# Optimization experiments

Measured on AMD Instinct MI355X. Metric: run time of the kernel, lower is better.

Reference implementation:

```python
import jax, jax.numpy as jnp
import numpy as np

B, T, C, H = 2, 2048, 1024, 16
HD = C // H
HID = C * 4 // 3  # 1365, SwiGLU hidden
EPS = 1e-5


def _ln(x, g, b):
    m = x.mean(-1, keepdims=True)
    v = ((x - m) ** 2).mean(-1, keepdims=True)
    return (x - m) / jnp.sqrt(v + EPS) * g + b


def setup_inputs() -> dict:
    key0 = jax.random.key(0)
    ks = jax.random.split(key0, 16)
    s = 0.02
    inp = {
        'query': jax.random.normal(ks[0], (B, T, C), jnp.float32),
        'key': jax.random.normal(ks[1], (B, T, C), jnp.float32),
        'g_q': jnp.ones((C,), jnp.float32), 'b_q': jnp.zeros((C,), jnp.float32),
        'g_k': jnp.ones((C,), jnp.float32), 'b_k': jnp.zeros((C,), jnp.float32),
        'in_proj_w': jax.random.normal(ks[2], (3 * C, C), jnp.float32) * s,
        'in_proj_b': jnp.zeros((3 * C,), jnp.float32),
        'out_w': jax.random.normal(ks[3], (C, C), jnp.float32) * s,
        'out_b': jnp.zeros((C,), jnp.float32),
        'proj_w': jax.random.normal(ks[4], (C, C), jnp.float32) * s,
        'proj_b': jnp.zeros((C,), jnp.float32),
        'rel_table': jax.random.normal(ks[5], (H, 2 * 2048 - 1), jnp.float32) * s,
        'g_ffn': jnp.ones((C,), jnp.float32), 'b_ffn': jnp.zeros((C,), jnp.float32),
        'w1': jax.random.normal(ks[6], (HID, C), jnp.float32) * s,
        'w2': jax.random.normal(ks[7], (HID, C), jnp.float32) * s,
        'w3': jax.random.normal(ks[8], (C, HID), jnp.float32) * s,
        'g_out': jnp.ones((C,), jnp.float32), 'b_out': jnp.zeros((C,), jnp.float32),
        'max_len': 2048,
    }
    return inp


def reference(query, key, g_q, b_q, g_k, b_k, in_proj_w, in_proj_b, out_w, out_b,
              proj_w, proj_b, rel_table, g_ffn, b_ffn, w1, w2, w3, g_out, b_out, max_len):
    Tq, Tk = query.shape[1], key.shape[1]
    q = _ln(query, g_q, b_q)
    k = _ln(key, g_k, b_k)
    # in-projection (torch MHA packed weights)
    wq, wk, wv = jnp.split(in_proj_w, 3, axis=0)
    bq, bk, bv = jnp.split(in_proj_b, 3, axis=0)
    qp = (q @ wq.T + bq).reshape(B, Tq, H, HD).transpose(0, 2, 1, 3)
    kp = (k @ wk.T + bk).reshape(B, Tk, H, HD).transpose(0, 2, 1, 3)
    vp = (k @ wv.T + bv).reshape(B, Tk, H, HD).transpose(0, 2, 1, 3)
    # relative-position bias, mean over heads -> [Tq,Tk] additive mask
    rel_idx = jnp.clip(jnp.arange(Tq)[:, None] - jnp.arange(Tk)[None, :] + (max_len - 1),
                       0, 2 * max_len - 2)
    mask = rel_table[:, rel_idx].mean(axis=0)  # [Tq,Tk]
    scores = jnp.einsum('bhqd,bhkd->bhqk', qp, kp) / jnp.sqrt(jnp.float32(HD))
    attn = jax.nn.softmax(scores + mask[None, None], axis=-1)
    ctx = jnp.einsum('bhqk,bhkd->bhqd', attn, vp)
    ctx = ctx.transpose(0, 2, 1, 3).reshape(B, Tq, C)
    attn_out = ctx @ out_w.T + out_b
    attn_out = attn_out @ proj_w.T + proj_b
    x = query + attn_out
    # SwiGLU FFN (proj dropout/dropout are identity at eval)
    h = _ln(x, g_ffn, b_ffn)
    ff = (jax.nn.silu(h @ w1.T) * (h @ w2.T)) @ w3.T
    x = x + ff
    return _ln(x, g_out, b_out)
```

## Files before the change

### kernel.cpp

```cpp
#include <hip/hip_runtime.h>
#include <hip/hip_bf16.h>

static constexpr int Bb  = 2;
static constexpr int Tt  = 2048;
static constexpr int Cc  = 1024;
static constexpr int Hh  = 16;
static constexpr int HDi = 64;
static constexpr int HID = 1365;
static constexpr int HIDP = 1408;
static constexpr int Mm  = Bb * Tt;

typedef unsigned short u16;
typedef __attribute__((ext_vector_type(8))) short bf16x8;
typedef __attribute__((ext_vector_type(4))) float f32x4;
typedef __attribute__((ext_vector_type(8))) unsigned short u16x8;
typedef __attribute__((ext_vector_type(4))) unsigned short u16x4;

__device__ inline u16 f2bf(float f) {
    unsigned u = __builtin_bit_cast(unsigned, f);
    u += 0x7fffu + ((u >> 16) & 1u);
    return (u16)(u >> 16);
}

__device__ inline unsigned cvtpk(float lo, float hi) {
    unsigned r;
    asm("v_cvt_pk_bf16_f32 %0, %1, %2" : "=v"(r) : "v"(lo), "v"(hi));
    return r;
}

__device__ inline float vexp2(float x) {
    float r;
    asm("v_exp_f32 %0, %1" : "=v"(r) : "v"(x));
    return r;
}

__device__ inline void gl16(const void* g, void* l) {
    __builtin_amdgcn_global_load_lds(
        (const __attribute__((address_space(1))) unsigned*)g,
        (__attribute__((address_space(3))) unsigned*)l, 16, 0, 0);
}

template<int OUTBF>
__global__ __launch_bounds__(256) void ln_k(const float* __restrict__ x,
                                            const float* __restrict__ g,
                                            const float* __restrict__ b,
                                            void* __restrict__ yv) {
    int row = blockIdx.x;
    int tid = threadIdx.x;
    const float4* xr = (const float4*)(x + (size_t)row * Cc);
    float4 v = xr[tid];
    float s  = v.x + v.y + v.z + v.w;
    float ss = v.x*v.x + v.y*v.y + v.z*v.z + v.w*v.w;
    __shared__ float rs[256], rq[256];
    rs[tid] = s; rq[tid] = ss;
    __syncthreads();
    for (int o = 128; o > 0; o >>= 1) {
        if (tid < o) { rs[tid] += rs[tid+o]; rq[tid] += rq[tid+o]; }
        __syncthreads();
    }
    float mean = rs[0] * (1.f/Cc);
    float var  = rq[0] * (1.f/Cc) - mean*mean;
    float inv  = rsqrtf(var + 1e-5f);
    float4 gv = ((const float4*)g)[tid];
    float4 bv = ((const float4*)b)[tid];
    float o0 = (v.x-mean)*inv*gv.x + bv.x;
    float o1 = (v.y-mean)*inv*gv.y + bv.y;
    float o2 = (v.z-mean)*inv*gv.z + bv.z;
    float o3 = (v.w-mean)*inv*gv.w + bv.w;
    if (OUTBF) {
        u16x4 o4 = { f2bf(o0), f2bf(o1), f2bf(o2), f2bf(o3) };
        ((u16x4*)((u16*)yv + (size_t)row * Cc))[tid] = o4;
    } else {
        float4 o4 = { o0, o1, o2, o3 };
        ((float4*)((float*)yv + (size_t)row * Cc))[tid] = o4;
    }
}

__global__ __launch_bounds__(256) void ln2_k(const float* __restrict__ q,
                                             const float* __restrict__ k,
                                             const float* __restrict__ gq, const float* __restrict__ bq,
                                             const float* __restrict__ gk, const float* __restrict__ bk,
                                             u16* __restrict__ qn, u16* __restrict__ kn) {
    int row = blockIdx.x;
    const float* x; const float* g; const float* bb; u16* y; int r;
    if (row < Mm) { x = q; g = gq; bb = bq; y = qn; r = row; }
    else          { x = k; g = gk; bb = bk; y = kn; r = row - Mm; }
    int tid = threadIdx.x;
    float4 v = ((const float4*)(x + (size_t)r * Cc))[tid];
    float s  = v.x + v.y + v.z + v.w;
    float ss = v.x*v.x + v.y*v.y + v.z*v.z + v.w*v.w;
    __shared__ float rs[256], rq2[256];
    rs[tid] = s; rq2[tid] = ss;
    __syncthreads();
    for (int o = 128; o > 0; o >>= 1) {
        if (tid < o) { rs[tid] += rs[tid+o]; rq2[tid] += rq2[tid+o]; }
        __syncthreads();
    }
    float mean = rs[0] * (1.f/Cc);
    float var  = rq2[0] * (1.f/Cc) - mean*mean;
    float inv  = rsqrtf(var + 1e-5f);
    float4 gv = ((const float4*)g)[tid];
    float4 bv = ((const float4*)bb)[tid];
    u16x4 o4 = { f2bf((v.x-mean)*inv*gv.x + bv.x), f2bf((v.y-mean)*inv*gv.y + bv.y),
                 f2bf((v.z-mean)*inv*gv.z + bv.z), f2bf((v.w-mean)*inv*gv.w + bv.w) };
    ((u16x4*)(y + (size_t)r * Cc))[tid] = o4;
}

__global__ __launch_bounds__(256) void meanrel_k(const float* __restrict__ rel,
                                                 float* __restrict__ mr) {
    int j = blockIdx.x * 256 + threadIdx.x;
    if (j < 2*Tt - 1) {
        float s = 0.f;
        #pragma unroll
        for (int h = 0; h < Hh; h++) s += rel[(size_t)h * (2*Tt - 1) + j];
        mr[j] = s * (1.f/Hh);
    }
}

__global__ __launch_bounds__(256) void cvt4_k(const float* __restrict__ s0, u16* __restrict__ d0, int n0,
                                              const float* __restrict__ s1, u16* __restrict__ d1, int n1,
                                              const float* __restrict__ s2, u16* __restrict__ d2, int n2, int v2,
                                              const float* __restrict__ s3, u16* __restrict__ d3, int n3, int v3) {
    int u = blockIdx.x * 256 + threadIdx.x;
    const float* src; u16* dst; int valid;
    if (u < n0)              { src = s0; dst = d0; valid = n0*8; }
    else if ((u -= n0) < n1) { src = s1; dst = d1; valid = n1*8; }
    else if ((u -= n1) < n2) { src = s2; dst = d2; valid = v2; }
    else if ((u -= n2) < n3) { src = s3; dst = d3; valid = v3; }
    else return;
    int e0 = u * 8;
    u16x8 o;
    if (e0 + 8 <= valid) {
        float4 a = *(const float4*)(src + e0);
        float4 b = *(const float4*)(src + e0 + 4);
        o[0]=f2bf(a.x); o[1]=f2bf(a.y); o[2]=f2bf(a.z); o[3]=f2bf(a.w);
        o[4]=f2bf(b.x); o[5]=f2bf(b.y); o[6]=f2bf(b.z); o[7]=f2bf(b.w);
    } else {
        #pragma unroll
        for (int j = 0; j < 8; j++) {
            int e = e0 + j;
            o[j] = f2bf(e < valid ? src[e] : 0.f);
        }
    }
    *(u16x8*)(dst + (size_t)e0) = o;
}

__global__ __launch_bounds__(256) void cvt_k(const float* __restrict__ src,
                                             u16* __restrict__ dst,
                                             int Rs, int Cs, int Cd, int total8) {
    int idx = blockIdx.x * 256 + threadIdx.x;
    if (idx >= total8) return;
    int e0 = idx * 8;
    int r = e0 / Cd, c0 = e0 - r * Cd;
    u16x8 o;
    #pragma unroll
    for (int j = 0; j < 8; j++) {
        int c = c0 + j;
        float v = (r < Rs && c < Cs) ? src[(size_t)r * Cs + c] : 0.f;
        o[j] = f2bf(v);
    }
    *(u16x8*)(dst + (size_t)e0) = o;
}

__global__ __launch_bounds__(256) void cvtT_k(const float* __restrict__ src,
                                              u16* __restrict__ dst) {
    __shared__ float t[64][65];
    int j0 = blockIdx.x * 64, c0 = blockIdx.y * 64;
    int tid = threadIdx.x;
    #pragma unroll
    for (int i = 0; i < 16; i++) {
        int e = tid + i*256;
        int c = e >> 6, j = e & 63;
        t[c][j] = src[(size_t)(c0 + c) * Cc + j0 + j];
    }
    __syncthreads();
    #pragma unroll
    for (int i = 0; i < 16; i++) {
        int e = tid + i*256;
        int j = e >> 6, c = e & 63;
        dst[(size_t)(j0 + j) * Cc + c0 + c] = f2bf(t[c][j]);
    }
}

__global__ __launch_bounds__(256) void bias_k(const float* __restrict__ wp,
                                              const float* __restrict__ bo,
                                              const float* __restrict__ bp,
                                              float* __restrict__ bc) {
    int i = blockIdx.x, tid = threadIdx.x;
    float4 w = ((const float4*)(wp + (size_t)i * Cc))[tid];
    float4 b = ((const float4*)bo)[tid];
    float s = w.x*b.x + w.y*b.y + w.z*b.z + w.w*b.w;
    __shared__ float red[256];
    red[tid] = s; __syncthreads();
    for (int o = 128; o > 0; o >>= 1) {
        if (tid < o) red[tid] += red[tid+o];
        __syncthreads();
    }
    if (tid == 0) bc[i] = red[0] + bp[i];
}

template<int OUTBF, int HASRES, int HASBIAS>
__global__ __launch_bounds__(256) void mgemm64_k(const u16* __restrict__ A,
                                                 const u16* __restrict__ W,
                                                 const float* __restrict__ bias,
                                                 const float* __restrict__ res,
                                                 void* __restrict__ outv,
                                                 int N, int K) {
    __shared__ u16 As[2][64*32];
    __shared__ u16 Ws[2][128*32];
    int bm = blockIdx.y * 64, bn = blockIdx.x * 128;
    int tid = threadIdx.x, w = tid >> 6, l = tid & 63;
    int lr = l & 15, lh = l >> 4;
    int wm = (w >> 1) * 32, wn = (w & 1) * 64;
    f32x4 acc[2][4] = {};

    auto stage = [&](int buf, int kt) {
        {
            int row = tid >> 2, slot = tid & 3;
            int ko = kt + ((slot ^ (row & 3)) << 3);
            gl16(A + (size_t)(bm + row) * K + ko, (char*)As[buf] + tid * 16);
        }
        #pragma unroll
        for (int c = 0; c < 2; c++) {
            int i = c*256 + tid;
            int row = i >> 2, slot = i & 3;
            int ko = kt + ((slot ^ (row & 3)) << 3);
            gl16(W + (size_t)(bn + row) * K + ko, (char*)Ws[buf] + (c*256 + tid) * 16);
        }
    };
    stage(0, 0);
    for (int kt = 0; kt < K; kt += 32) {
        int buf = (kt >> 5) & 1;
        __syncthreads();
        if (kt + 32 < K) stage(buf ^ 1, kt + 32);
        bf16x8 af[2], wf[4];
        #pragma unroll
        for (int f = 0; f < 2; f++) {
            int r = wm + f*16 + lr;
            af[f] = *(const bf16x8*)((const char*)As[buf] + r*64 + ((lh ^ (r & 3)) << 4));
        }
        #pragma unroll
        for (int f = 0; f < 4; f++) {
            int rn = wn + f*16 + lr;
            wf[f] = *(const bf16x8*)((const char*)Ws[buf] + rn*64 + ((lh ^ (rn & 3)) << 4));
        }
        #pragma unroll
        for (int fm = 0; fm < 2; fm++)
            #pragma unroll
            for (int fn = 0; fn < 4; fn++)
                acc[fm][fn] = __builtin_amdgcn_mfma_f32_16x16x32_bf16(af[fm], wf[fn], acc[fm][fn], 0, 0, 0);
    }

    #pragma unroll
    for (int fm = 0; fm < 2; fm++) {
        #pragma unroll
        for (int r = 0; r < 4; r++) {
            int row = bm + wm + fm*16 + lh*4 + r;
            #pragma unroll
            for (int fn = 0; fn < 4; fn++) {
                int col = bn + wn + fn*16 + lr;
                float v = acc[fm][fn][r];
                if (HASBIAS) v += bias[col];
                if (HASRES)  v += res[(size_t)row * N + col];
                if (OUTBF) ((u16*)outv)[(size_t)row * N + col] = f2bf(v);
                else       ((float*)outv)[(size_t)row * N + col] = v;
            }
        }
    }
}

__global__ __launch_bounds__(256) void mqkv_k(const u16* __restrict__ qn,
                                              const u16* __restrict__ kn,
                                              const u16* __restrict__ wA,
                                              const float* __restrict__ bias3,
                                              u16* __restrict__ out3) {
    int z = blockIdx.z;
    const u16* A = z ? kn : qn;
    const u16* W = wA + (size_t)z * Cc * Cc;
    const float* bias = bias3 + z * Cc;
    u16* out = out3 + (size_t)z * Mm * Cc;

    __shared__ u16 As[2][128*32];
    __shared__ u16 Ws[2][128*32];
    int bm = blockIdx.y * 128, bn = blockIdx.x * 128;
    int tid = threadIdx.x, w = tid >> 6, l = tid & 63;
    int lr = l & 15, lh = l >> 4;
    int wm = (w >> 1) * 64, wn = (w & 1) * 64;
    f32x4 acc[4][4] = {};

    auto stage = [&](int buf, int kt) {
        #pragma unroll
        for (int c = 0; c < 2; c++) {
            int i = w*128 + c*64 + l;
            int row = i >> 2, slot = i & 3;
            int ko = kt + ((slot ^ (row & 3)) << 3);
            gl16(A + (size_t)(bm + row) * Cc + ko, (char*)As[buf] + (w*128 + c*64) * 16);
            gl16(W + (size_t)(bn + row) * Cc + ko, (char*)Ws[buf] + (w*128 + c*64) * 16);
        }
    };
    stage(0, 0);
    for (int kt = 0; kt < Cc; kt += 32) {
        int buf = (kt >> 5) & 1;
        __syncthreads();
        if (kt + 32 < Cc) stage(buf ^ 1, kt + 32);
        bf16x8 af[4], wf[4];
        #pragma unroll
        for (int f = 0; f < 4; f++) {
            int r = wm + f*16 + lr;
            af[f] = *(const bf16x8*)((const char*)As[buf] + r*64 + ((lh ^ (r & 3)) << 4));
            int rn = wn + f*16 + lr;
            wf[f] = *(const bf16x8*)((const char*)Ws[buf] + rn*64 + ((lh ^ (rn & 3)) << 4));
        }
        #pragma unroll
        for (int fm = 0; fm < 4; fm++)
            #pragma unroll
            for (int fn = 0; fn < 4; fn++)
                acc[fm][fn] = __builtin_amdgcn_mfma_f32_16x16x32_bf16(af[fm], wf[fn], acc[fm][fn], 0, 0, 0);
    }

    #pragma unroll
    for (int fm = 0; fm < 4; fm++) {
        #pragma unroll
        for (int r = 0; r < 4; r++) {
            int row = bm + wm + fm*16 + lh*4 + r;
            #pragma unroll
            for (int fn = 0; fn < 4; fn++) {
                int col = bn + wn + fn*16 + lr;
                out[(size_t)row * Cc + col] = f2bf(acc[fm][fn][r] + bias[col]);
            }
        }
    }
}

__global__ __launch_bounds__(256) void mswiglu64_k(const u16* __restrict__ A,
                                                   const u16* __restrict__ W1,
                                                   const u16* __restrict__ W2,
                                                   u16* __restrict__ out,
                                                   int N, int K) {
    __shared__ u16 As[2][64*32];
    __shared__ u16 W1s[2][128*32];
    __shared__ u16 W2s[2][128*32];
    int bm = blockIdx.y * 64, bn = blockIdx.x * 128;
    int tid = threadIdx.x, w = tid >> 6, l = tid & 63;
    int lr = l & 15, lh = l >> 4;
    int wm = (w >> 1) * 32, wn = (w & 1) * 64;
    f32x4 acc1[2][4] = {};
    f32x4 acc2[2][4] = {};

    auto stage = [&](int buf, int kt) {
        {
            int row = tid >> 2, slot = tid & 3;
            int ko = kt + ((slot ^ (row & 3)) << 3);
            gl16(A + (size_t)(bm + row) * K + ko, (char*)As[buf] + tid * 16);
        }
        #pragma unroll
        for (int c = 0; c < 2; c++) {
            int i = c*256 + tid;
            int row = i >> 2, slot = i & 3;
            int ko = kt + ((slot ^ (row & 3)) << 3);
            gl16(W1 + (size_t)(bn + row) * K + ko, (char*)W1s[buf] + (c*256 + tid) * 16);
            gl16(W2 + (size_t)(bn + row) * K + ko, (char*)W2s[buf] + (c*256 + tid) * 16);
        }
    };
    stage(0, 0);
    for (int kt = 0; kt < K; kt += 32) {
        int buf = (kt >> 5) & 1;
        __syncthreads();
        if (kt + 32 < K) stage(buf ^ 1, kt + 32);
        bf16x8 af[2], w1f[4], w2f[4];
        #pragma unroll
        for (int f = 0; f < 2; f++) {
            int r = wm + f*16 + lr;
            af[f] = *(const bf16x8*)((const char*)As[buf] + r*64 + ((lh ^ (r & 3)) << 4));
        }
        #pragma unroll
        for (int f = 0; f < 4; f++) {
            int rn = wn + f*16 + lr;
            int offn = rn*64 + ((lh ^ (rn & 3)) << 4);
            w1f[f] = *(const bf16x8*)((const char*)W1s[buf] + offn);
            w2f[f] = *(const bf16x8*)((const char*)W2s[buf] + offn);
        }
        #pragma unroll
        for (int fm = 0; fm < 2; fm++)
            #pragma unroll
            for (int fn = 0; fn < 4; fn++) {
                acc1[fm][fn] = __builtin_amdgcn_mfma_f32_16x16x32_bf16(af[fm], w1f[fn], acc1[fm][fn], 0, 0, 0);
                acc2[fm][fn] = __builtin_amdgcn_mfma_f32_16x16x32_bf16(af[fm], w2f[fn], acc2[fm][fn], 0, 0, 0);
            }
    }

    #pragma unroll
    for (int fm = 0; fm < 2; fm++) {
        #pragma unroll
        for (int r = 0; r < 4; r++) {
            int row = bm + wm + fm*16 + lh*4 + r;
            #pragma unroll
            for (int fn = 0; fn < 4; fn++) {
                int col = bn + wn + fn*16 + lr;
                float a = acc1[fm][fn][r];
                float sig = 1.f / (1.f + __expf(-a));
                out[(size_t)row * N + col] = f2bf(a * sig * acc2[fm][fn][r]);
            }
        }
    }
}

__global__ __launch_bounds__(256) void vt_k(const u16* __restrict__ vp,
                                            u16* __restrict__ vt) {
    int blk = blockIdx.x;
    int bh = blk >> 5, kb = blk & 31;
    int b = bh >> 4, h = bh & 15;
    __shared__ u16 t[64][65];
    int tid = threadIdx.x;
    size_t bc = (size_t)b*Tt*Cc + (size_t)h*HDi;
    #pragma unroll
    for (int i = 0; i < 16; i++) {
        int e = tid + i*256;
        int k = e >> 6, d = e & 63;
        t[d][k] = vp[bc + (size_t)(kb*64 + k)*Cc + d];
    }
    __syncthreads();
    #pragma unroll
    for (int i = 0; i < 16; i++) {
        int e = tid + i*256;
        int d = e >> 6, k = e & 63;
        vt[((size_t)bh*64 + d)*Tt + kb*64 + k] = t[d][k];
    }
}

__global__ __launch_bounds__(512) void fattn_k(const u16* __restrict__ qp,
                                               const u16* __restrict__ kp,
                                               const u16* __restrict__ vt,
                                               const float* __restrict__ mr,
                                               u16* __restrict__ ctx) {
    __shared__ u16 Kt[2*4096];
    __shared__ u16 Vts[2*4096];
    __shared__ u16 Pt[8][1024];
    __shared__ float mrw[2176];

    constexpr float C1 = 0.18033688011118324f;

    int bid = blockIdx.x;
    int blk = ((bid & 7) << 6) | (bid >> 3);
    int qt = blk & 15, h = (blk >> 4) & 15, b = blk >> 8;
    int q0 = qt * 128;
    int tid = threadIdx.x, w = tid >> 6, l = tid & 63;
    int lr = l & 15, lh = l >> 4;
    size_t bc = (size_t)b * Tt * Cc + (size_t)h * HDi;
    const u16* vtb = vt + (size_t)(b*Hh + h) * HDi * Tt;

    for (int i = tid; i < 2175; i += 512) mrw[i] = mr[q0 + i] * 8.f;

    bf16x8 qa[2];
    {
        const u16* qrow = qp + bc + (size_t)(q0 + w*16 + lr) * Cc;
        qa[0] = *(const bf16x8*)(qrow + lh*8);
        qa[1] = *(const bf16x8*)(qrow + 32 + lh*8);
    }

    f32x4 oacc[4] = {};
    float mrun = -1e30f, lrun = 0.f;

    int ksw = (lr & 7) << 4;
    const char* pK0 = (const char*)Kt  + lr*128 + ((       lh*16) ^ ksw);
    const char* pK1 = (const char*)Kt  + lr*128 + ((64   + lh*16) ^ ksw);
    const char* pV0 = (const char*)Vts + lr*128 + ((       lh*16) ^ ksw);
    const char* pV1 = (const char*)Vts + lr*128 + ((64   + lh*16) ^ ksw);
    char* pw0 = (char*)Pt[w] + lr*128 + ((      lh*8) ^ ksw);
    char* pw1 = (char*)Pt[w] + lr*128 + ((32  + lh*8) ^ ksw);
    char* pw2 = (char*)Pt[w] + lr*128 + ((64  + lh*8) ^ ksw);
    char* pw3 = (char*)Pt[w] + lr*128 + ((96  + lh*8) ^ ksw);
    const char* pr0 = (const char*)Pt[w] + lr*128 + ((     lh*16) ^ ksw);
    const char* pr1 = (const char*)Pt[w] + lr*128 + ((64 + lh*16) ^ ksw);
    const char* pm = (const char*)mrw + (w*16 + lr - lh*4 + 2047 - 51) * 4;

    int sl = tid & 7, kr0 = tid >> 3;
    int so = (sl ^ (kr0 & 7)) << 3;
    const u16* gK = kp + bc + (size_t)kr0 * Cc + so;
    const u16* gV = vtb + (size_t)kr0 * Tt + so;
    int wb = (tid & 448) * 16;
    char* dK0 = (char*)Kt  + wb;
    char* dV0 = (char*)Vts + wb;

    auto stage = [&](int bufo) {
        gl16(gK, dK0 + bufo);
        gl16(gV, dV0 + bufo);
        gK += 64*Cc;
        gV += 64;
    };

    auto tile = [&](int bufo) {
        f32x4 s[4];
        #pragma unroll
        for (int f = 0; f < 4; f++) {
            s[f][0] = *(const float*)(pm + (51 - f*16    ) * 4);
            s[f][1] = *(const float*)(pm + (51 - f*16 - 1) * 4);
            s[f][2] = *(const float*)(pm + (51 - f*16 - 2) * 4);
            s[f][3] = *(const float*)(pm + (51 - f*16 - 3) * 4);
        }
        pm -= 256;
        __builtin_amdgcn_s_setprio(1);
        #pragma unroll
        for (int f = 0; f < 4; f++) {
            bf16x8 kb0 = *(const bf16x8*)(pK0 + bufo + f*2048);
            s[f] = __builtin_amdgcn_mfma_f32_16x16x32_bf16(kb0, qa[0], s[f], 0, 0, 0);
            bf16x8 kb1 = *(const bf16x8*)(pK1 + bufo + f*2048);
            s[f] = __builtin_amdgcn_mfma_f32_16x16x32_bf16(kb1, qa[1], s[f], 0, 0, 0);
        }
        __builtin_amdgcn_s_setprio(0);

        float tm = -1e30f;
        #pragma unroll
        for (int f = 0; f < 4; f++)
            #pragma unroll
            for (int r = 0; r < 4; r++) tm = fmaxf(tm, s[f][r]);
        tm = fmaxf(tm, __shfl_xor(tm, 16));
        tm = fmaxf(tm, __shfl_xor(tm, 32));

        float corr = 1.f;
        bool nod = __all(tm <= mrun + 64.f);
        if (!nod) {
            float mn = fmaxf(mrun, tm);
            corr = vexp2((mrun - mn) * C1);
            mrun = mn;
        }
        float mnc = mrun * C1;
        float ts = 0.f;
        #pragma unroll
        for (int f = 0; f < 4; f++)
            #pragma unroll
            for (int r = 0; r < 4; r++) {
                float e = vexp2(fmaf(s[f][r], C1, -mnc));
                s[f][r] = e; ts += e;
            }
        ts += __shfl_xor(ts, 16);
        ts += __shfl_xor(ts, 32);
        if (nod) {
            lrun += ts;
        } else {
            lrun = lrun*corr + ts;
            float cr0 = __shfl(corr, lh*4 + 0);
            float cr1 = __shfl(corr, lh*4 + 1);
            float cr2 = __shfl(corr, lh*4 + 2);
            float cr3 = __shfl(corr, lh*4 + 3);
            #pragma unroll
            for (int f = 0; f < 4; f++) {
                oacc[f][0] *= cr0; oacc[f][1] *= cr1;
                oacc[f][2] *= cr2; oacc[f][3] *= cr3;
            }
        }

        { uint2 p2 = { cvtpk(s[0][0], s[0][1]), cvtpk(s[0][2], s[0][3]) }; *(uint2*)pw0 = p2; }
        { uint2 p2 = { cvtpk(s[1][0], s[1][1]), cvtpk(s[1][2], s[1][3]) }; *(uint2*)pw1 = p2; }
        { uint2 p2 = { cvtpk(s[2][0], s[2][1]), cvtpk(s[2][2], s[2][3]) }; *(uint2*)pw2 = p2; }
        { uint2 p2 = { cvtpk(s[3][0], s[3][1]), cvtpk(s[3][2], s[3][3]) }; *(uint2*)pw3 = p2; }

        bf16x8 pa0 = *(const bf16x8*)pr0;
        bf16x8 pa1 = *(const bf16x8*)pr1;
        __builtin_amdgcn_s_setprio(1);
        #pragma unroll
        for (int f = 0; f < 4; f++) {
            bf16x8 vb0 = *(const bf16x8*)(pV0 + bufo + f*2048);
            oacc[f] = __builtin_amdgcn_mfma_f32_16x16x32_bf16(pa0, vb0, oacc[f], 0, 0, 0);
            bf16x8 vb1 = *(const bf16x8*)(pV1 + bufo + f*2048);
            oacc[f] = __builtin_amdgcn_mfma_f32_16x16x32_bf16(pa1, vb1, oacc[f], 0, 0, 0);
        }
        __builtin_amdgcn_s_setprio(0);
    };

    stage(0);
    #pragma unroll 1
    for (int kt = 0; kt < 32; kt += 2) {
        __syncthreads();
        stage(8192);
        tile(0);
        __syncthreads();
        if (kt < 30) stage(0);
        tile(8192);
    }

    float li0 = __shfl(lrun, lh*4 + 0);
    float li1 = __shfl(lrun, lh*4 + 1);
    float li2 = __shfl(lrun, lh*4 + 2);
    float li3 = __shfl(lrun, lh*4 + 3);
    float iv[4] = { 1.f/li0, 1.f/li1, 1.f/li2, 1.f/li3 };
    #pragma unroll
    for (int r = 0; r < 4; r++) {
        int row = q0 + w*16 + lh*4 + r;
        #pragma unroll
        for (int f = 0; f < 4; f++)
            ctx[bc + (size_t)row * Cc + f*16 + lr] = f2bf(oacc[f][r] * iv[r]);
    }
}

extern "C" void kernel_launch(void* const* d_in, const int* in_sizes, int n_in,
                              void* d_out, int out_size, void* d_ws, size_t ws_size,
                              hipStream_t stream) {
    const float* query     = (const float*)d_in[0];
    const float* key       = (const float*)d_in[1];
    const float* g_q       = (const float*)d_in[2];
    const float* b_q       = (const float*)d_in[3];
    const float* g_k       = (const float*)d_in[4];
    const float* b_k       = (const float*)d_in[5];
    const float* in_proj_w = (const float*)d_in[6];
    const float* in_proj_b = (const float*)d_in[7];
    const float* out_w     = (const float*)d_in[8];
    const float* out_b     = (const float*)d_in[9];
    const float* proj_w    = (const float*)d_in[10];
    const float* proj_b    = (const float*)d_in[11];
    const float* rel_table = (const float*)d_in[12];
    const float* g_ffn     = (const float*)d_in[13];
    const float* b_ffn     = (const float*)d_in[14];
    const float* w1        = (const float*)d_in[15];
    const float* w2        = (const float*)d_in[16];
    const float* w3        = (const float*)d_in[17];
    const float* g_out     = (const float*)d_in[18];
    const float* b_out     = (const float*)d_in[19];

    char* p = (char*)d_ws;
    auto alloc = [&](size_t bytes) { char* r = p; p += bytes; return r; };
    const size_t MCb = (size_t)Mm * Cc * 2;
    u16* wA  = (u16*)alloc((size_t)3*Cc*Cc*2);
    u16* wPb = (u16*)alloc((size_t)Cc*Cc*2);
    u16* wOt = (u16*)alloc((size_t)Cc*Cc*2);
    u16* wCb = (u16*)alloc((size_t)Cc*Cc*2);
    u16* w1b = (u16*)alloc((size_t)HIDP*Cc*2);
    u16* w2b = (u16*)alloc((size_t)HIDP*Cc*2);
    u16* w3b = (u16*)alloc((size_t)Cc*HIDP*2);
    float* bc = (float*)alloc(Cc*4);
    float* mr = (float*)alloc(4096*4);
    u16* qn = (u16*)alloc(MCb);
    u16* kn = (u16*)alloc(MCb);
    u16* qp = (u16*)alloc(MCb);
    u16* kp = (u16*)alloc(MCb);
    u16* vp = (u16*)alloc(MCb);
    u16* vt = (u16*)alloc(MCb);
    float* x  = (float*)alloc((size_t)Mm*Cc*4);
    float* x2 = (float*)alloc((size_t)Mm*Cc*4);
    u16* ctx = qn;
    u16* h   = qp;
    u16* gf  = vp;

    dim3 blk(256);
    {
        int n0 = 3*Cc*Cc/8;
        int n1 = Cc*Cc/8;
        int n2 = HIDP*Cc/8;
        int n3 = HIDP*Cc/8;
        int nblk = (n0 + n1 + n2 + n3) / 256;
        cvt4_k<<<nblk, blk, 0, stream>>>(in_proj_w, wA, n0,
                                         proj_w, wPb, n1,
                                         w1, w1b, n2, HID*Cc,
                                         w2, w2b, n3, HID*Cc);
    }
    cvt_k<<<(Cc*HIDP/8 + 255)/256, blk, 0, stream>>>(w3, w3b, Cc, HID, HIDP, Cc*HIDP/8);
    cvtT_k<<<dim3(16,16), blk, 0, stream>>>(out_w, wOt);
    mgemm64_k<1,0,0><<<dim3(Cc/128, Cc/64), blk, 0, stream>>>(wPb, wOt, nullptr, nullptr, wCb, Cc, Cc);
    bias_k<<<Cc, blk, 0, stream>>>(proj_w, out_b, proj_b, bc);
    meanrel_k<<<16, blk, 0, stream>>>(rel_table, mr);

    ln2_k<<<2*Mm, blk, 0, stream>>>(query, key, g_q, b_q, g_k, b_k, qn, kn);

    dim3 gqkv(Cc/128, Mm/128, 3);
    mqkv_k<<<gqkv, blk, 0, stream>>>(qn, kn, wA, in_proj_b, qp);

    vt_k<<<Bb*Hh*32, blk, 0, stream>>>(vp, vt);
    fattn_k<<<Bb*Hh*16, dim3(512), 0, stream>>>(qp, kp, vt, mr, ctx);

    dim3 g1(Cc/128, Mm/64);
    mgemm64_k<0,1,1><<<g1, blk, 0, stream>>>(ctx, wCb, bc, query, x, Cc, Cc);

    ln_k<1><<<Mm, blk, 0, stream>>>(x, g_ffn, b_ffn, h);
    dim3 g2(HIDP/128, Mm/64);
    mswiglu64_k<<<g2, blk, 0, stream>>>(h, w1b, w2b, gf, HIDP, Cc);
    dim3 g3(Cc/128, Mm/64);
    mgemm64_k<0,1,0><<<g3, blk, 0, stream>>>(gf, w3b, nullptr, x, x2, Cc, HIDP);

    ln_k<0><<<Mm, blk, 0, stream>>>(x2, g_out, b_out, d_out);
}
```

Measured before the change: 253.5 us.

## Fuse weight-prep kernels, fold weight-combine GEMM into QKV launch, keep P in registers

The six preprocessing kernels (weight casts, out_w transpose, bias combine, mean rel-bias) merge into one prep kernel with block-range dispatch. The proj_w·out_w combine GEMM becomes an extra z-slice of the QKV GEMM launch, so one more launch disappears. In flash attention, S is computed transposed with a new K shared-memory swizzle so softmax probabilities feed the PV MFMA straight from registers. This drops the shared-memory P round-trip, the per-row shuffles for correction and normalisation, and the scalar stores in favour of vector stores. The risk is more complex indexing and swizzle correctness in the attention kernel.

```diff
diff --git a/kernel.cpp b/kernel.cpp
--- a/kernel.cpp
+++ b/kernel.cpp
@@ -106,97 +106,83 @@
     ((u16x4*)(y + (size_t)r * Cc))[tid] = o4;
 }
 
-__global__ __launch_bounds__(256) void meanrel_k(const float* __restrict__ rel,
-                                                 float* __restrict__ mr) {
-    int j = blockIdx.x * 256 + threadIdx.x;
-    if (j < 2*Tt - 1) {
-        float s = 0.f;
-        #pragma unroll
-        for (int h = 0; h < Hh; h++) s += rel[(size_t)h * (2*Tt - 1) + j];
-        mr[j] = s * (1.f/Hh);
-    }
-}
-
-__global__ __launch_bounds__(256) void cvt4_k(const float* __restrict__ s0, u16* __restrict__ d0, int n0,
-                                              const float* __restrict__ s1, u16* __restrict__ d1, int n1,
-                                              const float* __restrict__ s2, u16* __restrict__ d2, int n2, int v2,
-                                              const float* __restrict__ s3, u16* __restrict__ d3, int n3, int v3) {
-    int u = blockIdx.x * 256 + threadIdx.x;
-    const float* src; u16* dst; int valid;
-    if (u < n0)              { src = s0; dst = d0; valid = n0*8; }
-    else if ((u -= n0) < n1) { src = s1; dst = d1; valid = n1*8; }
-    else if ((u -= n1) < n2) { src = s2; dst = d2; valid = v2; }
-    else if ((u -= n2) < n3) { src = s3; dst = d3; valid = v3; }
-    else return;
-    int e0 = u * 8;
-    u16x8 o;
-    if (e0 + 8 <= valid) {
-        float4 a = *(const float4*)(src + e0);
-        float4 b = *(const float4*)(src + e0 + 4);
-        o[0]=f2bf(a.x); o[1]=f2bf(a.y); o[2]=f2bf(a.z); o[3]=f2bf(a.w);
-        o[4]=f2bf(b.x); o[5]=f2bf(b.y); o[6]=f2bf(b.z); o[7]=f2bf(b.w);
+__global__ __launch_bounds__(256) void prep_k(const float* __restrict__ in_proj_w, u16* __restrict__ wA,
+                                              const float* __restrict__ proj_w,  u16* __restrict__ wPb,
+                                              const float* __restrict__ w1, u16* __restrict__ w1b,
+                                              const float* __restrict__ w2, u16* __restrict__ w2b,
+                                              const float* __restrict__ w3, u16* __restrict__ w3b,
+                                              const float* __restrict__ out_w, u16* __restrict__ wOt,
+                                              const float* __restrict__ out_b, const float* __restrict__ bp,
+                                              float* __restrict__ bc,
+                                              const float* __restrict__ rel, float* __restrict__ mr) {
+    __shared__ float sh[64*65];
+    int bid = blockIdx.x, tid = threadIdx.x;
+    if (bid < 3456) {
+        int u = bid * 256 + tid;
+        const float* src; u16* dst; int valid;
+        if (u < 1536*256)                   { src = in_proj_w; dst = wA;  valid = 3*Cc*Cc; }
+        else if ((u -= 1536*256) < 512*256) { src = proj_w;    dst = wPb; valid = Cc*Cc; }
+        else if ((u -= 512*256) < 704*256)  { src = w1;        dst = w1b; valid = HID*Cc; }
+        else     { u -= 704*256;              src = w2;        dst = w2b; valid = HID*Cc; }
+        int e0 = u * 8;
+        u16x8 o;
+        if (e0 + 8 <= valid) {
+            float4 a = *(const float4*)(src + e0);
+            float4 b = *(const float4*)(src + e0 + 4);
+            o[0]=f2bf(a.x); o[1]=f2bf(a.y); o[2]=f2bf(a.z); o[3]=f2bf(a.w);
+            o[4]=f2bf(b.x); o[5]=f2bf(b.y); o[6]=f2bf(b.z); o[7]=f2bf(b.w);
+        } else {
+            #pragma unroll
+            for (int j = 0; j < 8; j++) { int e = e0 + j; o[j] = f2bf(e < valid ? src[e] : 0.f); }
+        }
+        *(u16x8*)(dst + (size_t)e0) = o;
+    } else if (bid < 4160) {
+        int idx = (bid - 3456) * 256 + tid;
+        int e0 = idx * 8;
+        int r = e0 / HIDP, c0 = e0 - r * HIDP;
+        u16x8 o;
+        #pragma unroll
+        for (int j = 0; j < 8; j++) {
+            int c = c0 + j;
+            o[j] = f2bf(c < HID ? w3[(size_t)r * HID + c] : 0.f);
+        }
+        *(u16x8*)(w3b + (size_t)e0) = o;
+    } else if (bid < 4416) {
+        int id = bid - 4160;
+        int j0 = (id & 15) * 64, c0 = (id >> 4) * 64;
+        #pragma unroll
+        for (int i = 0; i < 16; i++) {
+            int e = tid + i*256;
+            int c = e >> 6, j = e & 63;
+            sh[c*65 + j] = out_w[(size_t)(c0 + c) * Cc + j0 + j];
+        }
+        __syncthreads();
+        #pragma unroll
+        for (int i = 0; i < 16; i++) {
+            int e = tid + i*256;
+            int j = e >> 6, c = e & 63;
+            wOt[(size_t)(j0 + j) * Cc + c0 + c] = f2bf(sh[c*65 + j]);
+        }
+    } else if (bid < 5440) {
+        int i = bid - 4416;
+        float4 w = ((const float4*)(proj_w + (size_t)i * Cc))[tid];
+        float4 b = ((const float4*)out_b)[tid];
+        float s = w.x*b.x + w.y*b.y + w.z*b.z + w.w*b.w;
+        sh[tid] = s; __syncthreads();
+        for (int o = 128; o > 0; o >>= 1) {
+            if (tid < o) sh[tid] += sh[tid+o];
+            __syncthreads();
+        }
+        if (tid == 0) bc[i] = sh[0] + bp[i];
     } else {
-        #pragma unroll
-        for (int j = 0; j < 8; j++) {
-            int e = e0 + j;
-            o[j] = f2bf(e < valid ? src[e] : 0.f);
-        }
-    }
-    *(u16x8*)(dst + (size_t)e0) = o;
-}
-
-__global__ __launch_bounds__(256) void cvt_k(const float* __restrict__ src,
-                                             u16* __restrict__ dst,
-                                             int Rs, int Cs, int Cd, int total8) {
-    int idx = blockIdx.x * 256 + threadIdx.x;
-    if (idx >= total8) return;
-    int e0 = idx * 8;
-    int r = e0 / Cd, c0 = e0 - r * Cd;
-    u16x8 o;
-    #pragma unroll
-    for (int j = 0; j < 8; j++) {
-        int c = c0 + j;
-        float v = (r < Rs && c < Cs) ? src[(size_t)r * Cs + c] : 0.f;
-        o[j] = f2bf(v);
-    }
-    *(u16x8*)(dst + (size_t)e0) = o;
-}
-
-__global__ __launch_bounds__(256) void cvtT_k(const float* __restrict__ src,
-                                              u16* __restrict__ dst) {
-    __shared__ float t[64][65];
-    int j0 = blockIdx.x * 64, c0 = blockIdx.y * 64;
-    int tid = threadIdx.x;
-    #pragma unroll
-    for (int i = 0; i < 16; i++) {
-        int e = tid + i*256;
-        int c = e >> 6, j = e & 63;
-        t[c][j] = src[(size_t)(c0 + c) * Cc + j0 + j];
-    }
-    __syncthreads();
-    #pragma unroll
-    for (int i = 0; i < 16; i++) {
-        int e = tid + i*256;
-        int j = e >> 6, c = e & 63;
-        dst[(size_t)(j0 + j) * Cc + c0 + c] = f2bf(t[c][j]);
-    }
-}
-
-__global__ __launch_bounds__(256) void bias_k(const float* __restrict__ wp,
-                                              const float* __restrict__ bo,
-                                              const float* __restrict__ bp,
-                                              float* __restrict__ bc) {
-    int i = blockIdx.x, tid = threadIdx.x;
-    float4 w = ((const float4*)(wp + (size_t)i * Cc))[tid];
-    float4 b = ((const float4*)bo)[tid];
-    float s = w.x*b.x + w.y*b.y + w.z*b.z + w.w*b.w;
-    __shared__ float red[256];
-    red[tid] = s; __syncthreads();
-    for (int o = 128; o > 0; o >>= 1) {
-        if (tid < o) red[tid] += red[tid+o];
-        __syncthreads();
-    }
-    if (tid == 0) bc[i] = red[0] + bp[i];
+        int j = (bid - 5440) * 256 + tid;
+        if (j < 2*Tt - 1) {
+            float s = 0.f;
+            #pragma unroll
+            for (int h = 0; h < Hh; h++) s += rel[(size_t)h * (2*Tt - 1) + j];
+            mr[j] = s * (1.f/Hh);
+        }
+    }
 }
 
 template<int OUTBF, int HASRES, int HASBIAS>
@@ -273,12 +259,14 @@
                                               const u16* __restrict__ kn,
                                               const u16* __restrict__ wA,
                                               const float* __restrict__ bias3,
-                                              u16* __restrict__ out3) {
+                                              u16* __restrict__ out3,
+                                              const u16* __restrict__ wPb,
+                                              const u16* __restrict__ wOt,
+                                              u16* __restrict__ wCb) {
     int z = blockIdx.z;
-    const u16* A = z ? kn : qn;
-    const u16* W = wA + (size_t)z * Cc * Cc;
-    const float* bias = bias3 + z * Cc;
-    u16* out = out3 + (size_t)z * Mm * Cc;
+    const u16* A; const u16* W; const float* bias = bias3; u16* out;
+    if (z < 3) { A = z ? kn : qn; W = wA + (size_t)z * Cc * Cc; bias = bias3 + z * Cc; out = out3 + (size_t)z * Mm * Cc; }
+    else       { if (blockIdx.y >= 8) return; A = wPb; W = wOt; out = wCb; }
 
     __shared__ u16 As[2][128*32];
     __shared__ u16 Ws[2][128*32];
@@ -326,7 +314,9 @@
             #pragma unroll
             for (int fn = 0; fn < 4; fn++) {
                 int col = bn + wn + fn*16 + lr;
-                out[(size_t)row * Cc + col] = f2bf(acc[fm][fn][r] + bias[col]);
+                float v = acc[fm][fn][r];
+                if (z < 3) v += bias[col];
+                out[(size_t)row * Cc + col] = f2bf(v);
             }
         }
     }
@@ -433,9 +423,8 @@
                                                const u16* __restrict__ vt,
                                                const float* __restrict__ mr,
                                                u16* __restrict__ ctx) {
-    __shared__ u16 Kt[2*4096];
-    __shared__ u16 Vts[2*4096];
-    __shared__ u16 Pt[8][1024];
+    __shared__ alignas(128) u16 Kt[2*4096];
+    __shared__ alignas(128) u16 Vts[2*4096];
     __shared__ float mrw[2176];
 
     constexpr float C1 = 0.18033688011118324f;
@@ -461,21 +450,16 @@
     f32x4 oacc[4] = {};
     float mrun = -1e30f, lrun = 0.f;
 
-    int ksw = (lr & 7) << 4;
-    const char* pK0 = (const char*)Kt  + lr*128 + ((       lh*16) ^ ksw);
-    const char* pK1 = (const char*)Kt  + lr*128 + ((64   + lh*16) ^ ksw);
-    const char* pV0 = (const char*)Vts + lr*128 + ((       lh*16) ^ ksw);
-    const char* pV1 = (const char*)Vts + lr*128 + ((64   + lh*16) ^ ksw);
-    char* pw0 = (char*)Pt[w] + lr*128 + ((      lh*8) ^ ksw);
-    char* pw1 = (char*)Pt[w] + lr*128 + ((32  + lh*8) ^ ksw);
-    char* pw2 = (char*)Pt[w] + lr*128 + ((64  + lh*8) ^ ksw);
-    char* pw3 = (char*)Pt[w] + lr*128 + ((96  + lh*8) ^ ksw);
-    const char* pr0 = (const char*)Pt[w] + lr*128 + ((     lh*16) ^ ksw);
-    const char* pr1 = (const char*)Pt[w] + lr*128 + ((64 + lh*16) ^ ksw);
-    const char* pm = (const char*)mrw + (w*16 + lr - lh*4 + 2047 - 51) * 4;
+    const char* pKb0 = (const char*)Kt + (lr>>2)*1024 + (lr&3)*128
+                       + ((lh ^ (lr & 3)) << 4) + (((lr >> 2) & 1) << 6);
+    const char* pKb1 = (const char*)((size_t)pKb0 ^ 64);
+    int g6 = ((((lr >> 2) ^ (lr >> 3)) & 1) << 6);
+    const char* pV0 = (const char*)Vts + lr*128 + ((lh ^ (lr & 3)) << 4) + g6;
+    const char* pV1 = (const char*)((size_t)pV0 ^ 64);
+    const char* pm = (const char*)mrw + (w*16 + lr - lh*8 + 2047 - 39) * 4;
 
     int sl = tid & 7, kr0 = tid >> 3;
-    int so = (sl ^ (kr0 & 7)) << 3;
+    int so = (sl ^ (kr0 & 7) ^ (((kr0 >> 3) & 1) << 2)) << 3;
     const u16* gK = kp + bc + (size_t)kr0 * Cc + so;
     const u16* gV = vtb + (size_t)kr0 * Tt + so;
     int wb = (tid & 448) * 16;
@@ -493,19 +477,26 @@
         f32x4 s[4];
         #pragma unroll
         for (int f = 0; f < 4; f++) {
-            s[f][0] = *(const float*)(pm + (51 - f*16    ) * 4);
-            s[f][1] = *(const float*)(pm + (51 - f*16 - 1) * 4);
-            s[f][2] = *(const float*)(pm + (51 - f*16 - 2) * 4);
-            s[f][3] = *(const float*)(pm + (51 - f*16 - 3) * 4);
+            int ob = 39 - (f & 1)*32 - (f >> 1)*4;
+            s[f][0] = *(const float*)(pm + (ob    ) * 4);
+            s[f][1] = *(const float*)(pm + (ob - 1) * 4);
+            s[f][2] = *(const float*)(pm + (ob - 2) * 4);
+            s[f][3] = *(const float*)(pm + (ob - 3) * 4);
         }
         pm -= 256;
         __builtin_amdgcn_s_setprio(1);
-        #pragma unroll
-        for (int f = 0; f < 4; f++) {
-            bf16x8 kb0 = *(const bf16x8*)(pK0 + bufo + f*2048);
-            s[f] = __builtin_amdgcn_mfma_f32_16x16x32_bf16(kb0, qa[0], s[f], 0, 0, 0);
-            bf16x8 kb1 = *(const bf16x8*)(pK1 + bufo + f*2048);
-            s[f] = __builtin_amdgcn_mfma_f32_16x16x32_bf16(kb1, qa[1], s[f], 0, 0, 0);
+        {
+            const char* k0 = pKb0 + bufo;
+            const char* k1 = pKb1 + bufo;
+            bf16x8 kb;
+            kb = *(const bf16x8*)(k0 + 0);    s[0] = __builtin_amdgcn_mfma_f32_16x16x32_bf16(kb, qa[0], s[0], 0, 0, 0);
+            kb = *(const bf16x8*)(k1 + 0);    s[0] = __builtin_amdgcn_mfma_f32_16x16x32_bf16(kb, qa[1], s[0], 0, 0, 0);
+            kb = *(const bf16x8*)(k0 + 4096); s[1] = __builtin_amdgcn_mfma_f32_16x16x32_bf16(kb, qa[0], s[1], 0, 0, 0);
+            kb = *(const bf16x8*)(k1 + 4096); s[1] = __builtin_amdgcn_mfma_f32_16x16x32_bf16(kb, qa[1], s[1], 0, 0, 0);
+            kb = *(const bf16x8*)(k1 + 512);  s[2] = __builtin_amdgcn_mfma_f32_16x16x32_bf16(kb, qa[0], s[2], 0, 0, 0);
+            kb = *(const bf16x8*)(k0 + 512);  s[2] = __builtin_amdgcn_mfma_f32_16x16x32_bf16(kb, qa[1], s[2], 0, 0, 0);
+            kb = *(const bf16x8*)(k1 + 4608); s[3] = __builtin_amdgcn_mfma_f32_16x16x32_bf16(kb, qa[0], s[3], 0, 0, 0);
+            kb = *(const bf16x8*)(k0 + 4608); s[3] = __builtin_amdgcn_mfma_f32_16x16x32_bf16(kb, qa[1], s[3], 0, 0, 0);
         }
         __builtin_amdgcn_s_setprio(0);
 
@@ -539,31 +530,27 @@
             lrun += ts;
         } else {
             lrun = lrun*corr + ts;
-            float cr0 = __shfl(corr, lh*4 + 0);
-            float cr1 = __shfl(corr, lh*4 + 1);
-            float cr2 = __shfl(corr, lh*4 + 2);
-            float cr3 = __shfl(corr, lh*4 + 3);
             #pragma unroll
             for (int f = 0; f < 4; f++) {
-                oacc[f][0] *= cr0; oacc[f][1] *= cr1;
-                oacc[f][2] *= cr2; oacc[f][3] *= cr3;
+                oacc[f][0] *= corr; oacc[f][1] *= corr;
+                oacc[f][2] *= corr; oacc[f][3] *= corr;
             }
         }
 
-        { uint2 p2 = { cvtpk(s[0][0], s[0][1]), cvtpk(s[0][2], s[0][3]) }; *(uint2*)pw0 = p2; }
-        { uint2 p2 = { cvtpk(s[1][0], s[1][1]), cvtpk(s[1][2], s[1][3]) }; *(uint2*)pw1 = p2; }
-        { uint2 p2 = { cvtpk(s[2][0], s[2][1]), cvtpk(s[2][2], s[2][3]) }; *(uint2*)pw2 = p2; }
-        { uint2 p2 = { cvtpk(s[3][0], s[3][1]), cvtpk(s[3][2], s[3][3]) }; *(uint2*)pw3 = p2; }
-
-        bf16x8 pa0 = *(const bf16x8*)pr0;
-        bf16x8 pa1 = *(const bf16x8*)pr1;
+        uint4 pb0u = { cvtpk(s[0][0], s[0][1]), cvtpk(s[0][2], s[0][3]),
+                       cvtpk(s[2][0], s[2][1]), cvtpk(s[2][2], s[2][3]) };
+        uint4 pb1u = { cvtpk(s[1][0], s[1][1]), cvtpk(s[1][2], s[1][3]),
+                       cvtpk(s[3][0], s[3][1]), cvtpk(s[3][2], s[3][3]) };
+        bf16x8 pb0 = __builtin_bit_cast(bf16x8, pb0u);
+        bf16x8 pb1 = __builtin_bit_cast(bf16x8, pb1u);
+
         __builtin_amdgcn_s_setprio(1);
         #pragma unroll
         for (int f = 0; f < 4; f++) {
             bf16x8 vb0 = *(const bf16x8*)(pV0 + bufo + f*2048);
-            oacc[f] = __builtin_amdgcn_mfma_f32_16x16x32_bf16(pa0, vb0, oacc[f], 0, 0, 0);
+            oacc[f] = __builtin_amdgcn_mfma_f32_16x16x32_bf16(vb0, pb0, oacc[f], 0, 0, 0);
             bf16x8 vb1 = *(const bf16x8*)(pV1 + bufo + f*2048);
-            oacc[f] = __builtin_amdgcn_mfma_f32_16x16x32_bf16(pa1, vb1, oacc[f], 0, 0, 0);
+            oacc[f] = __builtin_amdgcn_mfma_f32_16x16x32_bf16(vb1, pb1, oacc[f], 0, 0, 0);
         }
         __builtin_amdgcn_s_setprio(0);
     };
@@ -579,17 +566,13 @@
         tile(8192);
     }
 
-    float li0 = __shfl(lrun, lh*4 + 0);
-    float li1 = __shfl(lrun, lh*4 + 1);
-    float li2 = __shfl(lrun, lh*4 + 2);
-    float li3 = __shfl(lrun, lh*4 + 3);
-    float iv[4] = { 1.f/li0, 1.f/li1, 1.f/li2, 1.f/li3 };
+    float iv = 1.f / lrun;
+    size_t rowoff = bc + (size_t)(q0 + w*16 + lr) * Cc;
     #pragma unroll
-    for (int r = 0; r < 4; r++) {
-        int row = q0 + w*16 + lh*4 + r;
-        #pragma unroll
-        for (int f = 0; f < 4; f++)
-            ctx[bc + (size_t)row * Cc + f*16 + lr] = f2bf(oacc[f][r] * iv[r]);
+    for (int f = 0; f < 4; f++) {
+        u16x4 o4 = { f2bf(oacc[f][0]*iv), f2bf(oacc[f][1]*iv),
+                     f2bf(oacc[f][2]*iv), f2bf(oacc[f][3]*iv) };
+        *(u16x4*)(ctx + rowoff + f*16 + lh*4) = o4;
     }
 }
 
@@ -642,27 +625,13 @@
     u16* gf  = vp;
 
     dim3 blk(256);
-    {
-        int n0 = 3*Cc*Cc/8;
-        int n1 = Cc*Cc/8;
-        int n2 = HIDP*Cc/8;
-        int n3 = HIDP*Cc/8;
-        int nblk = (n0 + n1 + n2 + n3) / 256;
-        cvt4_k<<<nblk, blk, 0, stream>>>(in_proj_w, wA, n0,
-                                         proj_w, wPb, n1,
-                                         w1, w1b, n2, HID*Cc,
-                                         w2, w2b, n3, HID*Cc);
-    }
-    cvt_k<<<(Cc*HIDP/8 + 255)/256, blk, 0, stream>>>(w3, w3b, Cc, HID, HIDP, Cc*HIDP/8);
-    cvtT_k<<<dim3(16,16), blk, 0, stream>>>(out_w, wOt);
-    mgemm64_k<1,0,0><<<dim3(Cc/128, Cc/64), blk, 0, stream>>>(wPb, wOt, nullptr, nullptr, wCb, Cc, Cc);
-    bias_k<<<Cc, blk, 0, stream>>>(proj_w, out_b, proj_b, bc);
-    meanrel_k<<<16, blk, 0, stream>>>(rel_table, mr);
+    prep_k<<<5456, blk, 0, stream>>>(in_proj_w, wA, proj_w, wPb, w1, w1b, w2, w2b,
+                                     w3, w3b, out_w, wOt, out_b, proj_b, bc, rel_table, mr);
 
     ln2_k<<<2*Mm, blk, 0, stream>>>(query, key, g_q, b_q, g_k, b_k, qn, kn);
 
-    dim3 gqkv(Cc/128, Mm/128, 3);
-    mqkv_k<<<gqkv, blk, 0, stream>>>(qn, kn, wA, in_proj_b, qp);
+    dim3 gqkv(Cc/128, Mm/128, 4);
+    mqkv_k<<<gqkv, blk, 0, stream>>>(qn, kn, wA, in_proj_b, qp, wPb, wOt, wCb);
 
     vt_k<<<Bb*Hh*32, blk, 0, stream>>>(vp, vt);
     fattn_k<<<Bb*Hh*16, dim3(512), 0, stream>>>(qp, kp, vt, mr, ctx);
```

After: 256.9 us. Within noise of the previous version (+1.4%).
